# Performance work log

Measured on AMD Instinct MI355X. Metric: run time of the kernel, lower is better.

The kernel has to match this reference:

```python
import jax, jax.numpy as jnp
import numpy as np


def setup_inputs() -> dict:
    key = jax.random.key(0)
    k1, k2, k3 = jax.random.split(key, 3)
    B, L, D, H = 8, 1024, 768, 128
    text = jax.random.normal(k1, (B, L, D), dtype=jnp.float32)
    mask = jnp.ones((B, L), dtype=jnp.float32)  # accepted by forward but unused
    # nn.Linear-style init scale
    W0 = jax.random.normal(k2, (H, D), dtype=jnp.float32) / np.sqrt(D)
    b0 = jnp.zeros((H,), dtype=jnp.float32)
    W1 = jax.random.normal(k3, (1, 2 * H), dtype=jnp.float32) / np.sqrt(2 * H)
    b1 = jnp.zeros((1,), dtype=jnp.float32)
    return {"text": text, "mask": mask, "W0": W0, "b0": b0, "W1": W1, "b1": b1}


def reference(text, mask, W0, b0, W1, b1):
    # h = relu(linear0(text))  -> [B, L, 128]
    h = jax.nn.relu(jnp.einsum('bld,hd->blh', text, W0) + b0)
    H = W0.shape[0]
    # linear([h_i ; h_j]) = h_i @ w_a + h_j @ w_b + b  (split the 256->1 weight)
    w_a = W1[0, :H]   # weights applied to the row (i) copy
    w_b = W1[0, H:]   # weights applied to the column (j) copy
    s1 = jnp.einsum('blh,h->bl', h, w_a)  # [B, L]
    s2 = jnp.einsum('blh,h->bl', h, w_b)  # [B, L]
    # logits[b, i, j] = sigmoid(s1[b, i] + s2[b, j] + b1)
    logits = jax.nn.sigmoid(s1[:, :, None] + s2[:, None, :] + b1[0])
    return logits
```

## Files before the change

### kernel.cpp

```cpp
#include <hip/hip_runtime.h>

#define M_ROWS 8192
#define DIM    768
#define HCH    128
#define KSTEPS 24

typedef __bf16 bf16x8 __attribute__((ext_vector_type(8)));
typedef float  f32x4  __attribute__((ext_vector_type(4)));

__global__ __launch_bounds__(256) void convert_w0_frag(
    const float* __restrict__ W0, bf16x8* __restrict__ W0f)
{
    const int g    = blockIdx.x * 256 + threadIdx.x;
    const int c    = g / (KSTEPS * 64);
    const int r    = g - c * (KSTEPS * 64);
    const int s    = r >> 6;
    const int lane = r & 63;
    const int n16  = lane & 15;
    const int quad = lane >> 4;
    const float* src = W0 + (size_t)(c * 16 + n16) * DIM + s * 32 + quad * 8;
    float4 v0 = *(const float4*)src;
    float4 v1 = *(const float4*)(src + 4);
    bf16x8 o;
    o[0] = (__bf16)v0.x; o[1] = (__bf16)v0.y; o[2] = (__bf16)v0.z; o[3] = (__bf16)v0.w;
    o[4] = (__bf16)v1.x; o[5] = (__bf16)v1.y; o[6] = (__bf16)v1.z; o[7] = (__bf16)v1.w;
    W0f[g] = o;
}

__global__ __launch_bounds__(256) void gemm_s_kernel(
    const float* __restrict__ text,
    const bf16x8* __restrict__ W0f,
    const float* __restrict__ b0,
    const float* __restrict__ W1,
    float* __restrict__ s1, float* __restrict__ s2)
{
    __shared__ float red1[16][4];
    __shared__ float red2[16][4];

    const int tid  = threadIdx.x;
    const int lane = tid & 63;
    const int wave = tid >> 6;
    const int n16  = lane & 15;
    const int quad = lane >> 4;
    const int row0 = blockIdx.x * 16;
    const int c0   = wave * 2;

    const float*  aptr  = text + (size_t)(row0 + n16) * DIM + quad * 8;
    const bf16x8* bptr0 = W0f + (size_t)(c0    ) * KSTEPS * 64 + lane;
    const bf16x8* bptr1 = W0f + (size_t)(c0 + 1) * KSTEPS * 64 + lane;

    f32x4 acc0 = (f32x4){0.f, 0.f, 0.f, 0.f};
    f32x4 acc1 = (f32x4){0.f, 0.f, 0.f, 0.f};

    float4 a0[3], a1[3];
    bf16x8 bv0[3], bv1[3];
    #pragma unroll
    for (int s = 0; s < 2; ++s) {
        a0[s]  = *(const float4*)(aptr + s * 32);
        a1[s]  = *(const float4*)(aptr + s * 32 + 4);
        bv0[s] = bptr0[s * 64];
        bv1[s] = bptr1[s * 64];
    }

    #pragma unroll
    for (int s = 0; s < KSTEPS; ++s) {
        const int sl = s % 3;
        const int pl = (s + 2) % 3;
        const int sp = (s + 2 < KSTEPS) ? (s + 2) : (s + 2 - KSTEPS);
        a0[pl]  = *(const float4*)(aptr + sp * 32);
        a1[pl]  = *(const float4*)(aptr + sp * 32 + 4);
        bv0[pl] = bptr0[sp * 64];
        bv1[pl] = bptr1[sp * 64];

        bf16x8 af;
        af[0] = (__bf16)a0[sl].x; af[1] = (__bf16)a0[sl].y;
        af[2] = (__bf16)a0[sl].z; af[3] = (__bf16)a0[sl].w;
        af[4] = (__bf16)a1[sl].x; af[5] = (__bf16)a1[sl].y;
        af[6] = (__bf16)a1[sl].z; af[7] = (__bf16)a1[sl].w;
        acc0 = __builtin_amdgcn_mfma_f32_16x16x32_bf16(af, bv0[sl], acc0, 0, 0, 0);
        acc1 = __builtin_amdgcn_mfma_f32_16x16x32_bf16(af, bv1[sl], acc1, 0, 0, 0);
    }

    float p1[4] = {0.f, 0.f, 0.f, 0.f};
    float p2[4] = {0.f, 0.f, 0.f, 0.f};
    #pragma unroll
    for (int j = 0; j < 2; ++j) {
        const f32x4 aj = j ? acc1 : acc0;
        const int col = wave * 32 + j * 16 + n16;
        const float bb = b0[col];
        const float wa = W1[col];
        const float wb = W1[HCH + col];
        #pragma unroll
        for (int r = 0; r < 4; ++r) {
            float h = aj[r] + bb;
            h = fmaxf(h, 0.f);
            p1[r] += h * wa;
            p2[r] += h * wb;
        }
    }
    #pragma unroll
    for (int r = 0; r < 4; ++r) {
        #pragma unroll
        for (int m = 8; m >= 1; m >>= 1) {
            p1[r] += __shfl_xor(p1[r], m);
            p2[r] += __shfl_xor(p2[r], m);
        }
    }
    if (n16 == 0) {
        #pragma unroll
        for (int r = 0; r < 4; ++r) {
            const int rr = quad * 4 + r;
            red1[rr][wave] = p1[r];
            red2[rr][wave] = p2[r];
        }
    }
    __syncthreads();
    if (tid < 16) {
        s1[row0 + tid] = red1[tid][0] + red1[tid][1] + red1[tid][2] + red1[tid][3];
        s2[row0 + tid] = red2[tid][0] + red2[tid][1] + red2[tid][2] + red2[tid][3];
    }
}

__global__ __launch_bounds__(256) void outer_sigmoid_kernel(
    const float* __restrict__ s1, const float* __restrict__ s2,
    const float* __restrict__ b1, float* __restrict__ out)
{
    const int bi = blockIdx.x;
    const int b  = bi >> 10;
    const float base = s1[bi] + b1[0];
    const float4 t = ((const float4*)(s2 + (b << 10)))[threadIdx.x];
    float4 r;
    r.x = 1.f / (1.f + __expf(-(base + t.x)));
    r.y = 1.f / (1.f + __expf(-(base + t.y)));
    r.z = 1.f / (1.f + __expf(-(base + t.z)));
    r.w = 1.f / (1.f + __expf(-(base + t.w)));
    ((float4*)out)[((size_t)bi << 8) + threadIdx.x] = r;
}

extern "C" void kernel_launch(void* const* d_in, const int* in_sizes, int n_in,
                              void* d_out, int out_size, void* d_ws, size_t ws_size,
                              hipStream_t stream)
{
    const float* text = (const float*)d_in[0];
    const float* W0 = (const float*)d_in[2];
    const float* b0 = (const float*)d_in[3];
    const float* W1 = (const float*)d_in[4];
    const float* b1 = (const float*)d_in[5];
    float* out = (float*)d_out;

    bf16x8* W0f = (bf16x8*)d_ws;
    float* s1 = (float*)((char*)d_ws + (size_t)HCH * DIM * sizeof(unsigned short));
    float* s2 = s1 + M_ROWS;

    convert_w0_frag<<<48, 256, 0, stream>>>(W0, W0f);
    gemm_s_kernel<<<512, 256, 0, stream>>>(text, W0f, b0, W1, s1, s2);
    outer_sigmoid_kernel<<<8192, 256, 0, stream>>>(s1, s2, b1, out);
}
```

Baseline: 102.5 us.

## Fuse weight conversion, GEMM and outer sigmoid into one persistent kernel

Result: slower. 204.1 us (+99.0%).

```diff
diff --git a/kernel.cpp b/kernel.cpp
--- a/kernel.cpp
+++ b/kernel.cpp
@@ -4,38 +4,39 @@
 #define DIM    768
 #define HCH    128
 #define KSTEPS 24
+#define NBLK   512
 
 typedef __bf16 bf16x8 __attribute__((ext_vector_type(8)));
 typedef float  f32x4  __attribute__((ext_vector_type(4)));
 
-__global__ __launch_bounds__(256) void convert_w0_frag(
-    const float* __restrict__ W0, bf16x8* __restrict__ W0f)
-{
-    const int g    = blockIdx.x * 256 + threadIdx.x;
-    const int c    = g / (KSTEPS * 64);
-    const int r    = g - c * (KSTEPS * 64);
-    const int s    = r >> 6;
-    const int lane = r & 63;
-    const int n16  = lane & 15;
-    const int quad = lane >> 4;
-    const float* src = W0 + (size_t)(c * 16 + n16) * DIM + s * 32 + quad * 8;
-    float4 v0 = *(const float4*)src;
-    float4 v1 = *(const float4*)(src + 4);
-    bf16x8 o;
-    o[0] = (__bf16)v0.x; o[1] = (__bf16)v0.y; o[2] = (__bf16)v0.z; o[3] = (__bf16)v0.w;
-    o[4] = (__bf16)v1.x; o[5] = (__bf16)v1.y; o[6] = (__bf16)v1.z; o[7] = (__bf16)v1.w;
-    W0f[g] = o;
+__device__ __forceinline__ void grid_arrive_wait(unsigned int* ctr, unsigned int target) {
+    __syncthreads();
+    if (threadIdx.x == 0) {
+        __threadfence();
+        __hip_atomic_fetch_add(ctr, 1u, __ATOMIC_ACQ_REL, __HIP_MEMORY_SCOPE_AGENT);
+        long long guard = 0;
+        while (__hip_atomic_load(ctr, __ATOMIC_ACQUIRE, __HIP_MEMORY_SCOPE_AGENT) < target) {
+            if (++guard > (1LL << 30)) break;
+            __builtin_amdgcn_s_sleep(2);
+        }
+    }
+    __syncthreads();
 }
 
-__global__ __launch_bounds__(256) void gemm_s_kernel(
+__global__ __launch_bounds__(256) void fused_all_kernel(
     const float* __restrict__ text,
-    const bf16x8* __restrict__ W0f,
+    const float* __restrict__ W0,
     const float* __restrict__ b0,
     const float* __restrict__ W1,
-    float* __restrict__ s1, float* __restrict__ s2)
+    const float* __restrict__ b1,
+    bf16x8* __restrict__ W0f,
+    float* __restrict__ s1, float* __restrict__ s2,
+    unsigned int* __restrict__ ctr,
+    float* __restrict__ out)
 {
     __shared__ float red1[16][4];
     __shared__ float red2[16][4];
+    __shared__ float s2s[1024];
 
     const int tid  = threadIdx.x;
     const int lane = tid & 63;
@@ -43,98 +44,123 @@
     const int n16  = lane & 15;
     const int quad = lane >> 4;
     const int row0 = blockIdx.x * 16;
-    const int c0   = wave * 2;
 
-    const float*  aptr  = text + (size_t)(row0 + n16) * DIM + quad * 8;
-    const bf16x8* bptr0 = W0f + (size_t)(c0    ) * KSTEPS * 64 + lane;
-    const bf16x8* bptr1 = W0f + (size_t)(c0 + 1) * KSTEPS * 64 + lane;
+    if (tid == 0) atomicCAS(ctr, 0xAAAAAAAAu, 0u);
 
-    f32x4 acc0 = (f32x4){0.f, 0.f, 0.f, 0.f};
-    f32x4 acc1 = (f32x4){0.f, 0.f, 0.f, 0.f};
+    {
+        const int g = blockIdx.x * 256 + tid;
+        if (g < 8 * KSTEPS * 64) {
+            const int c  = g / (KSTEPS * 64);
+            const int r  = g - c * (KSTEPS * 64);
+            const int s  = r >> 6;
+            const int l  = r & 63;
+            const float* src = W0 + (size_t)(c * 16 + (l & 15)) * DIM + s * 32 + (l >> 4) * 8;
+            float4 v0 = *(const float4*)src;
+            float4 v1 = *(const float4*)(src + 4);
+            bf16x8 o;
+            o[0] = (__bf16)v0.x; o[1] = (__bf16)v0.y; o[2] = (__bf16)v0.z; o[3] = (__bf16)v0.w;
+            o[4] = (__bf16)v1.x; o[5] = (__bf16)v1.y; o[6] = (__bf16)v1.z; o[7] = (__bf16)v1.w;
+            W0f[g] = o;
+        }
+    }
+    grid_arrive_wait(ctr, NBLK);
 
-    float4 a0[3], a1[3];
-    bf16x8 bv0[3], bv1[3];
-    #pragma unroll
-    for (int s = 0; s < 2; ++s) {
-        a0[s]  = *(const float4*)(aptr + s * 32);
-        a1[s]  = *(const float4*)(aptr + s * 32 + 4);
-        bv0[s] = bptr0[s * 64];
-        bv1[s] = bptr1[s * 64];
-    }
+    {
+        const int c0 = wave * 2;
+        const float*  aptr  = text + (size_t)(row0 + n16) * DIM + quad * 8;
+        const bf16x8* bptr0 = W0f + (size_t)(c0    ) * KSTEPS * 64 + lane;
+        const bf16x8* bptr1 = W0f + (size_t)(c0 + 1) * KSTEPS * 64 + lane;
 
-    #pragma unroll
-    for (int s = 0; s < KSTEPS; ++s) {
-        const int sl = s % 3;
-        const int pl = (s + 2) % 3;
-        const int sp = (s + 2 < KSTEPS) ? (s + 2) : (s + 2 - KSTEPS);
-        a0[pl]  = *(const float4*)(aptr + sp * 32);
-        a1[pl]  = *(const float4*)(aptr + sp * 32 + 4);
-        bv0[pl] = bptr0[sp * 64];
-        bv1[pl] = bptr1[sp * 64];
+        f32x4 acc0 = (f32x4){0.f, 0.f, 0.f, 0.f};
+        f32x4 acc1 = (f32x4){0.f, 0.f, 0.f, 0.f};
 
-        bf16x8 af;
-        af[0] = (__bf16)a0[sl].x; af[1] = (__bf16)a0[sl].y;
-        af[2] = (__bf16)a0[sl].z; af[3] = (__bf16)a0[sl].w;
-        af[4] = (__bf16)a1[sl].x; af[5] = (__bf16)a1[sl].y;
-        af[6] = (__bf16)a1[sl].z; af[7] = (__bf16)a1[sl].w;
-        acc0 = __builtin_amdgcn_mfma_f32_16x16x32_bf16(af, bv0[sl], acc0, 0, 0, 0);
-        acc1 = __builtin_amdgcn_mfma_f32_16x16x32_bf16(af, bv1[sl], acc1, 0, 0, 0);
-    }
+        float4 a0[3], a1[3];
+        bf16x8 bv0[3], bv1[3];
+        #pragma unroll
+        for (int s = 0; s < 2; ++s) {
+            a0[s]  = *(const float4*)(aptr + s * 32);
+            a1[s]  = *(const float4*)(aptr + s * 32 + 4);
+            bv0[s] = bptr0[s * 64];
+            bv1[s] = bptr1[s * 64];
+        }
 
-    float p1[4] = {0.f, 0.f, 0.f, 0.f};
-    float p2[4] = {0.f, 0.f, 0.f, 0.f};
-    #pragma unroll
-    for (int j = 0; j < 2; ++j) {
-        const f32x4 aj = j ? acc1 : acc0;
-        const int col = wave * 32 + j * 16 + n16;
-        const float bb = b0[col];
-        const float wa = W1[col];
-        const float wb = W1[HCH + col];
+        #pragma unroll
+        for (int s = 0; s < KSTEPS; ++s) {
+            const int sl = s % 3;
+            const int pl = (s + 2) % 3;
+            const int sp = (s + 2 < KSTEPS) ? (s + 2) : (s + 2 - KSTEPS);
+            a0[pl]  = *(const float4*)(aptr + sp * 32);
+            a1[pl]  = *(const float4*)(aptr + sp * 32 + 4);
+            bv0[pl] = bptr0[sp * 64];
+            bv1[pl] = bptr1[sp * 64];
+
+            bf16x8 af;
+            af[0] = (__bf16)a0[sl].x; af[1] = (__bf16)a0[sl].y;
+            af[2] = (__bf16)a0[sl].z; af[3] = (__bf16)a0[sl].w;
+            af[4] = (__bf16)a1[sl].x; af[5] = (__bf16)a1[sl].y;
+            af[6] = (__bf16)a1[sl].z; af[7] = (__bf16)a1[sl].w;
+            acc0 = __builtin_amdgcn_mfma_f32_16x16x32_bf16(af, bv0[sl], acc0, 0, 0, 0);
+            acc1 = __builtin_amdgcn_mfma_f32_16x16x32_bf16(af, bv1[sl], acc1, 0, 0, 0);
+        }
+
+        float p1[4] = {0.f, 0.f, 0.f, 0.f};
+        float p2[4] = {0.f, 0.f, 0.f, 0.f};
+        #pragma unroll
+        for (int j = 0; j < 2; ++j) {
+            const f32x4 aj = j ? acc1 : acc0;
+            const int col = wave * 32 + j * 16 + n16;
+            const float bb = b0[col];
+            const float wa = W1[col];
+            const float wb = W1[HCH + col];
+            #pragma unroll
+            for (int r = 0; r < 4; ++r) {
+                float h = aj[r] + bb;
+                h = fmaxf(h, 0.f);
+                p1[r] += h * wa;
+                p2[r] += h * wb;
+            }
+        }
         #pragma unroll
         for (int r = 0; r < 4; ++r) {
-            float h = aj[r] + bb;
-            h = fmaxf(h, 0.f);
-            p1[r] += h * wa;
-            p2[r] += h * wb;
+            #pragma unroll
+            for (int m = 8; m >= 1; m >>= 1) {
+                p1[r] += __shfl_xor(p1[r], m);
+                p2[r] += __shfl_xor(p2[r], m);
+            }
+        }
+        if (n16 == 0) {
+            #pragma unroll
+            for (int r = 0; r < 4; ++r) {
+                const int rr = quad * 4 + r;
+                red1[rr][wave] = p1[r];
+                red2[rr][wave] = p2[r];
+            }
+        }
+        __syncthreads();
+        if (tid < 16) {
+            s1[row0 + tid] = red1[tid][0] + red1[tid][1] + red1[tid][2] + red1[tid][3];
+            s2[row0 + tid] = red2[tid][0] + red2[tid][1] + red2[tid][2] + red2[tid][3];
         }
     }
-    #pragma unroll
-    for (int r = 0; r < 4; ++r) {
-        #pragma unroll
-        for (int m = 8; m >= 1; m >>= 1) {
-            p1[r] += __shfl_xor(p1[r], m);
-            p2[r] += __shfl_xor(p2[r], m);
+    grid_arrive_wait(ctr, 2 * NBLK);
+
+    {
+        const int b = row0 >> 10;
+        ((float4*)s2s)[tid] = ((const float4*)(s2 + (b << 10)))[tid];
+        const float bias = b1[0];
+        __syncthreads();
+        const float4 t = ((const float4*)s2s)[tid];
+        #pragma unroll 4
+        for (int r = 0; r < 16; ++r) {
+            const float base = s1[row0 + r] + bias;
+            float4 o;
+            o.x = 1.f / (1.f + __expf(-(base + t.x)));
+            o.y = 1.f / (1.f + __expf(-(base + t.y)));
+            o.z = 1.f / (1.f + __expf(-(base + t.z)));
+            o.w = 1.f / (1.f + __expf(-(base + t.w)));
+            ((float4*)out)[(size_t)(row0 + r) * 256 + tid] = o;
         }
     }
-    if (n16 == 0) {
-        #pragma unroll
-        for (int r = 0; r < 4; ++r) {
-            const int rr = quad * 4 + r;
-            red1[rr][wave] = p1[r];
-            red2[rr][wave] = p2[r];
-        }
-    }
-    __syncthreads();
-    if (tid < 16) {
-        s1[row0 + tid] = red1[tid][0] + red1[tid][1] + red1[tid][2] + red1[tid][3];
-        s2[row0 + tid] = red2[tid][0] + red2[tid][1] + red2[tid][2] + red2[tid][3];
-    }
-}
-
-__global__ __launch_bounds__(256) void outer_sigmoid_kernel(
-    const float* __restrict__ s1, const float* __restrict__ s2,
-    const float* __restrict__ b1, float* __restrict__ out)
-{
-    const int bi = blockIdx.x;
-    const int b  = bi >> 10;
-    const float base = s1[bi] + b1[0];
-    const float4 t = ((const float4*)(s2 + (b << 10)))[threadIdx.x];
-    float4 r;
-    r.x = 1.f / (1.f + __expf(-(base + t.x)));
-    r.y = 1.f / (1.f + __expf(-(base + t.y)));
-    r.z = 1.f / (1.f + __expf(-(base + t.z)));
-    r.w = 1.f / (1.f + __expf(-(base + t.w)));
-    ((float4*)out)[((size_t)bi << 8) + threadIdx.x] = r;
 }
 
 extern "C" void kernel_launch(void* const* d_in, const int* in_sizes, int n_in,
@@ -148,11 +174,11 @@
     const float* b1 = (const float*)d_in[5];
     float* out = (float*)d_out;
 
-    bf16x8* W0f = (bf16x8*)d_ws;
-    float* s1 = (float*)((char*)d_ws + (size_t)HCH * DIM * sizeof(unsigned short));
-    float* s2 = s1 + M_ROWS;
+    bf16x8*       W0f = (bf16x8*)d_ws;
+    float*        s1  = (float*)((char*)d_ws + 192 * 1024);
+    float*        s2  = s1 + M_ROWS;
+    unsigned int* ctr = (unsigned int*)((char*)d_ws + 256 * 1024);
 
-    convert_w0_frag<<<48, 256, 0, stream>>>(W0, W0f);
-    gemm_s_kernel<<<512, 256, 0, stream>>>(text, W0f, b0, W1, s1, s2);
-    outer_sigmoid_kernel<<<8192, 256, 0, stream>>>(s1, s2, b1, out);
+    fused_all_kernel<<<NBLK, 256, 0, stream>>>(text, W0, b0, W1, b1,
+                                               W0f, s1, s2, ctr, out);
 }
```
